# Kernel tuning notes

Hardware: AMD Instinct MI355X
Metric: run time of the kernel (lower is better)

Reference implementation:

```python
import jax, jax.numpy as jnp
import numpy as np

B, S, P, L, H = 64, 512, 32, 30, 768
FH = 1024  # fc_hidden_size


def setup_inputs() -> dict:
    key = jax.random.key(0)
    ks = jax.random.split(key, 8)
    token_embeddings = jax.random.normal(ks[0], (B, S, H), jnp.float32)
    pooler_output = jax.random.normal(ks[1], (B, H), jnp.float32)
    num_positions = jax.random.randint(ks[2], (B, P), 0, S)
    # labels: 0/1 codes, with trailing slots per example padded with -1 rows
    lab = jax.random.randint(ks[3], (B, P, L), 0, 2).astype(jnp.float32)
    valid = jax.random.randint(ks[4], (B, 1), 8, P + 1)  # num real slots per example
    row = jnp.arange(P)[None, :]
    lab = jnp.where((row < valid)[:, :, None], lab, -1.0)
    num_codes_labels = lab.reshape(B, P * L)
    W1 = jax.random.normal(ks[5], (2 * H, FH), jnp.float32) / np.sqrt(2 * H)
    b1 = jnp.zeros((FH,), jnp.float32)
    W2 = jax.random.normal(ks[6], (FH, FH // 2), jnp.float32) / np.sqrt(FH)
    b2 = jnp.zeros((FH // 2,), jnp.float32)
    W3 = jax.random.normal(ks[7], (FH // 2, L), jnp.float32) / np.sqrt(FH // 2)
    b3 = jnp.zeros((L,), jnp.float32)
    return {"token_embeddings": token_embeddings, "pooler_output": pooler_output,
            "num_positions": num_positions, "num_codes_labels": num_codes_labels,
            "W1": W1, "b1": b1, "W2": W2, "b2": b2, "W3": W3, "b3": b3}


def reference(token_embeddings, pooler_output, num_positions, num_codes_labels,
              W1, b1, W2, b2, W3, b3):
    # gather number-token hidden states: [B, P, H]
    p_hidden = jnp.take_along_axis(token_embeddings, num_positions[:, :, None], axis=1)
    feat = jnp.concatenate(
        [p_hidden, jnp.broadcast_to(pooler_output[:, None, :], p_hidden.shape)], axis=-1)
    # Batch_Net_CLS head. NOTE: original uses nn.LeakyReLU(True) -> negative_slope=1.0,
    # which is mathematically the identity, so the activations are omitted (faithful).
    h = feat @ W1 + b1
    h = h @ W2 + b2
    logits = h @ W3 + b3  # [B, P, L]

    labels = num_codes_labels.reshape(B, -1, L)
    pad_pre = jnp.any(labels != -1.0, axis=-1)  # [B, P] True for real slots
    mf = pad_pre.astype(jnp.float32)

    # BCEWithLogitsLoss over non-pad elements: softplus(x) - x*y, mean
    bce_elem = jax.nn.softplus(logits) - logits * labels
    bce_loss = jnp.sum(bce_elem * mf[:, :, None]) / (jnp.sum(mf) * L)

    binary = (jax.nn.sigmoid(logits) > 0.5).astype(jnp.float32)
    count_out = jnp.sum(binary, axis=-1)
    count_lab = jnp.sum(labels, axis=-1)
    count_loss = jnp.mean((count_out - count_lab) ** 2 * mf)

    # position loss: only slots where both counts are exactly 1 (single-hot)
    eq = (count_out == 1.0) & (count_lab == 1.0)
    pos_out = jnp.argmax(binary, axis=-1).astype(jnp.float32)
    pos_lab = jnp.argmax(labels, axis=-1).astype(jnp.float32)
    n_eq = jnp.sum(eq.astype(jnp.float32))
    pos_sum = jnp.sum((pos_out - pos_lab) ** 2 * eq.astype(jnp.float32))
    position_loss = jnp.where(n_eq > 0, pos_sum / jnp.maximum(n_eq, 1.0), 0.0)

    return bce_loss + 10.0 * count_loss + 5.0 * position_loss
```

## Files before the change

### kernel.cpp

```cpp
#include <hip/hip_runtime.h>
#include <cstddef>
#include <cstdint>

#define Mq   2048
#define Lq   30
#define N1q  1024
#define N2q  512
#define K1q  1536
#define Hq   768
#define NBLK 512

typedef float    f32x4 __attribute__((ext_vector_type(4)));
typedef _Float16 f16x8 __attribute__((ext_vector_type(8)));

#define GLD16(gptr, lptr) \
  __builtin_amdgcn_global_load_lds((const __attribute__((address_space(1))) void*)(gptr), \
                                   (__attribute__((address_space(3))) void*)(lptr), 16, 0, 0)

__device__ void transpose_tile(const float* __restrict__ src,
                               _Float16* __restrict__ dst,
                               int K, int N, int k0, int n0) {
  __shared__ float T[64][65];
  const int t = threadIdx.x;
  {
    const int kl = t >> 2, nc = (t & 3) * 16;
    const float* s = src + (size_t)(k0 + kl) * N + n0 + nc;
    float4 v0 = *(const float4*)s;
    float4 v1 = *(const float4*)(s + 4);
    float4 v2 = *(const float4*)(s + 8);
    float4 v3 = *(const float4*)(s + 12);
    T[nc + 0][kl] = v0.x; T[nc + 1][kl] = v0.y; T[nc + 2][kl] = v0.z; T[nc + 3][kl] = v0.w;
    T[nc + 4][kl] = v1.x; T[nc + 5][kl] = v1.y; T[nc + 6][kl] = v1.z; T[nc + 7][kl] = v1.w;
    T[nc + 8][kl] = v2.x; T[nc + 9][kl] = v2.y; T[nc +10][kl] = v2.z; T[nc +11][kl] = v2.w;
    T[nc +12][kl] = v3.x; T[nc +13][kl] = v3.y; T[nc +14][kl] = v3.z; T[nc +15][kl] = v3.w;
  }
  __syncthreads();
  {
    const int nl = t >> 2, kc = (t & 3) * 16;
    __align__(16) _Float16 tmp[16];
    #pragma unroll
    for (int i = 0; i < 16; ++i) tmp[i] = (_Float16)T[nl][kc + i];
    _Float16* d = dst + (size_t)(n0 + nl) * K + k0 + kc;
    *(uint4*)d       = *(const uint4*)tmp;
    *(uint4*)(d + 8) = *(const uint4*)(tmp + 8);
  }
}

__global__ __launch_bounds__(256)
void prep_all(const float* __restrict__ tok, const float* __restrict__ pool,
              const int* __restrict__ npos, const float* __restrict__ W1,
              const float* __restrict__ W2, const float* __restrict__ W3,
              _Float16* __restrict__ A1, _Float16* __restrict__ W1T,
              _Float16* __restrict__ W2T, float* __restrict__ W3T) {
  const int bid = blockIdx.x, tid = threadIdx.x;
  if (bid < 256) {
    const int q = tid >> 5, l32 = tid & 31;
    const int m = bid * 8 + q;
    const int bI = m >> 5, p = m & 31;
    const int pos = npos[bI * 32 + p];
    const float* src1 = tok + ((size_t)bI * 512 + pos) * Hq;
    const float* src2 = pool + (size_t)bI * Hq;
    _Float16* dst = A1 + (size_t)m * K1q;
    for (int g = l32; g < 384; g += 32) {
      const float* s = (g < 192) ? (src1 + g * 4) : (src2 + (g - 192) * 4);
      float4 v = *(const float4*)s;
      __align__(8) _Float16 o[4] = {(_Float16)v.x, (_Float16)v.y, (_Float16)v.z, (_Float16)v.w};
      *(uint2*)(dst + g * 4) = *(const uint2*)o;
    }
  } else if (bid < 640) {
    const int idx = bid - 256;
    transpose_tile(W1, W1T, K1q, N1q, (idx / 16) * 64, (idx % 16) * 64);
  } else if (bid < 768) {
    const int idx = bid - 640;
    transpose_tile(W2, W2T, N1q, N2q, (idx / 8) * 64, (idx % 8) * 64);
  } else {
    const int g = (bid - 768) * 256 + tid;
    for (int idx = g; idx < N2q * Lq; idx += 16 * 256) {
      const int k = idx / Lq, c = idx - k * Lq;
      W3T[(size_t)c * N2q + k] = W3[idx];
    }
  }
}

__global__ __launch_bounds__(256)
void gemm1_k(const _Float16* __restrict__ A, const _Float16* __restrict__ BT,
             const float* __restrict__ b1, _Float16* __restrict__ C1) {
  __shared__ _Float16 As[2][64 * 64];
  __shared__ _Float16 Bs[2][64 * 64];
  const int tid = threadIdx.x, w = tid >> 6, lane = tid & 63;
  const int n0 = blockIdx.x * 64, m0 = blockIdx.y * 64;
  const int ml = lane & 15, g4 = lane >> 4;
  const int wm = (w >> 1) * 32, wn = (w & 1) * 32;
  const int lr = lane >> 3, lc = lane & 7;

  f32x4 acc[2][2];
  #pragma unroll
  for (int i = 0; i < 2; ++i)
    #pragma unroll
    for (int j = 0; j < 2; ++j)
      #pragma unroll
      for (int r = 0; r < 4; ++r) acc[i][j][r] = 0.f;

  auto stage = [&](int it, int b) {
    const int kt = it * 64;
    #pragma unroll
    for (int t = 0; t < 2; ++t) {
      const int r  = w * 16 + t * 8 + lr;
      const int cs = lc ^ (r & 7);
      GLD16(A  + (size_t)(m0 + r) * K1q + kt + cs * 8, &As[b][(w * 16 + t * 8) * 64]);
      GLD16(BT + (size_t)(n0 + r) * K1q + kt + cs * 8, &Bs[b][(w * 16 + t * 8) * 64]);
    }
  };

  stage(0, 0);
  __syncthreads();
  #pragma unroll 1
  for (int it = 0; it < 24; ++it) {
    const int cur = it & 1;
    if (it < 23) stage(it + 1, cur ^ 1);
    f16x8 af[2][2], bf[2][2];
    #pragma unroll
    for (int i = 0; i < 2; ++i) {
      const int ar = wm + i * 16 + ml;
      const int br = wn + i * 16 + ml;
      #pragma unroll
      for (int ks = 0; ks < 2; ++ks) {
        af[i][ks] = *(const f16x8*)&As[cur][ar * 64 + (((ks * 4 + g4) ^ (ar & 7)) << 3)];
        bf[i][ks] = *(const f16x8*)&Bs[cur][br * 64 + (((ks * 4 + g4) ^ (br & 7)) << 3)];
      }
    }
    #pragma unroll
    for (int i = 0; i < 2; ++i)
      #pragma unroll
      for (int j = 0; j < 2; ++j)
        #pragma unroll
        for (int ks = 0; ks < 2; ++ks)
          acc[i][j] = __builtin_amdgcn_mfma_f32_16x16x32_f16(bf[j][ks], af[i][ks], acc[i][j], 0, 0, 0);
    __syncthreads();
  }

  #pragma unroll
  for (int i = 0; i < 2; ++i) {
    const int row = m0 + wm + i * 16 + ml;
    #pragma unroll
    for (int j = 0; j < 2; ++j) {
      const int col = n0 + wn + j * 16 + g4 * 4;
      const float4 bv = *(const float4*)(b1 + col);
      __align__(8) _Float16 o[4] = {(_Float16)(acc[i][j][0] + bv.x),
                                    (_Float16)(acc[i][j][1] + bv.y),
                                    (_Float16)(acc[i][j][2] + bv.z),
                                    (_Float16)(acc[i][j][3] + bv.w)};
      *(uint2*)(C1 + (size_t)row * N1q + col) = *(const uint2*)o;
    }
  }
}

__global__ __launch_bounds__(256)
void gemm2_k(const _Float16* __restrict__ A, const _Float16* __restrict__ BT,
             const float* __restrict__ b2, float* __restrict__ C2) {
  __shared__ _Float16 As[2][32 * 64];
  __shared__ _Float16 Bs[2][64 * 64];
  const int tid = threadIdx.x, w = tid >> 6, lane = tid & 63;
  const int n0 = blockIdx.x * 64, m0 = blockIdx.y * 32;
  const int ml = lane & 15, g4 = lane >> 4;
  const int wm = (w & 1) * 16, wn = (w >> 1) * 32;
  const int lr = lane >> 3, lc = lane & 7;

  f32x4 acc[2];
  #pragma unroll
  for (int j = 0; j < 2; ++j)
    #pragma unroll
    for (int r = 0; r < 4; ++r) acc[j][r] = 0.f;

  auto stage = [&](int it, int b) {
    const int kt = it * 64;
    {
      const int r  = w * 8 + lr;
      const int cs = lc ^ (r & 7);
      GLD16(A + (size_t)(m0 + r) * N1q + kt + cs * 8, &As[b][(w * 8) * 64]);
    }
    #pragma unroll
    for (int t = 0; t < 2; ++t) {
      const int r  = w * 16 + t * 8 + lr;
      const int cs = lc ^ (r & 7);
      GLD16(BT + (size_t)(n0 + r) * N1q + kt + cs * 8, &Bs[b][(w * 16 + t * 8) * 64]);
    }
  };

  stage(0, 0);
  __syncthreads();
  #pragma unroll 1
  for (int it = 0; it < 16; ++it) {
    const int cur = it & 1;
    if (it < 15) stage(it + 1, cur ^ 1);
    f16x8 af[2], bf[2][2];
    {
      const int ar = wm + ml;
      #pragma unroll
      for (int ks = 0; ks < 2; ++ks)
        af[ks] = *(const f16x8*)&As[cur][ar * 64 + (((ks * 4 + g4) ^ (ar & 7)) << 3)];
    }
    #pragma unroll
    for (int j = 0; j < 2; ++j) {
      const int br = wn + j * 16 + ml;
      #pragma unroll
      for (int ks = 0; ks < 2; ++ks)
        bf[j][ks] = *(const f16x8*)&Bs[cur][br * 64 + (((ks * 4 + g4) ^ (br & 7)) << 3)];
    }
    #pragma unroll
    for (int j = 0; j < 2; ++j)
      #pragma unroll
      for (int ks = 0; ks < 2; ++ks)
        acc[j] = __builtin_amdgcn_mfma_f32_16x16x32_f16(bf[j][ks], af[ks], acc[j], 0, 0, 0);
    __syncthreads();
  }

  const int row = m0 + wm + ml;
  #pragma unroll
  for (int j = 0; j < 2; ++j) {
    const int col = n0 + wn + j * 16 + g4 * 4;
    const float4 bv = *(const float4*)(b2 + col);
    float4 o;
    o.x = acc[j][0] + bv.x; o.y = acc[j][1] + bv.y;
    o.z = acc[j][2] + bv.z; o.w = acc[j][3] + bv.w;
    *(float4*)(C2 + (size_t)row * N2q + col) = o;
  }
}

__global__ __launch_bounds__(256)
void loss_kernel(const float* __restrict__ C2, const float* __restrict__ W3T,
                 const float* __restrict__ b3, const float* __restrict__ labels,
                 float* __restrict__ part) {
  __shared__ float hrow[4][512];
  __shared__ float red[4][5];
  const int tid = threadIdx.x, w = tid >> 6, lane = tid & 63;
  const int m = blockIdx.x * 4 + w;

  {
    const int k = lane * 8;
    const float* cp = C2 + (size_t)m * N2q + k;
    *(float4*)&hrow[w][k]     = *(const float4*)cp;
    *(float4*)&hrow[w][k + 4] = *(const float4*)(cp + 4);
  }
  __syncthreads();

  const int c  = lane & 31;
  const int kh = lane >> 5;
  float a0 = 0.f, a1 = 0.f, a2 = 0.f, a3 = 0.f;
  if (c < Lq) {
    const float* hp = hrow[w] + kh * 256;
    const float* wp = W3T + (size_t)c * N2q + kh * 256;
    #pragma unroll 4
    for (int i = 0; i < 256; i += 4) {
      const float4 wv = *(const float4*)(wp + i);
      a0 = fmaf(hp[i],     wv.x, a0);
      a1 = fmaf(hp[i + 1], wv.y, a1);
      a2 = fmaf(hp[i + 2], wv.z, a2);
      a3 = fmaf(hp[i + 3], wv.w, a3);
    }
  }
  float a = (a0 + a1) + (a2 + a3);
  a += __shfl_xor(a, 32);

  const bool act = lane < Lq;
  float logit = 0.f, lab = 0.f;
  if (act) {
    logit = a + b3[lane];
    lab = labels[(size_t)m * Lq + lane];
  }

  const unsigned long long validmask = __ballot(act && lab != -1.0f);
  const unsigned long long outmask   = __ballot(act && logit > 0.0f);
  const unsigned long long labmask   = __ballot(act && lab == 1.0f);
  const bool valid = (validmask != 0ULL);
  const int count_out = __popcll(outmask);
  const int count_lab = __popcll(labmask);

  float bce = 0.f;
  if (act && valid) {
    const float x = logit;
    bce = fmaxf(x, 0.f) + log1pf(expf(-fabsf(x))) - x * lab;
  }
  bce += __shfl_xor(bce, 16); bce += __shfl_xor(bce, 8);
  bce += __shfl_xor(bce, 4);  bce += __shfl_xor(bce, 2);
  bce += __shfl_xor(bce, 1);

  if (lane == 0) {
    float pb = 0.f, pv = 0.f, pc = 0.f, pe = 0.f, pp = 0.f;
    if (valid) {
      pb = bce; pv = 1.f;
      const float d = (float)count_out - (float)count_lab;
      pc = d * d;
    }
    if (count_out == 1 && count_lab == 1) {
      const float po = (float)(__ffsll((long long)outmask) - 1);
      const float pl = (float)(__ffsll((long long)labmask) - 1);
      pe = 1.f;
      const float dp = po - pl;
      pp = dp * dp;
    }
    red[w][0] = pb; red[w][1] = pv; red[w][2] = pc; red[w][3] = pe; red[w][4] = pp;
  }
  __syncthreads();
  if (tid < 5) {
    part[blockIdx.x * 5 + tid] =
        red[0][tid] + red[1][tid] + red[2][tid] + red[3][tid];
  }
}

__global__ __launch_bounds__(256)
void finalize_kernel(const float* __restrict__ part, float* __restrict__ out) {
  __shared__ float red[32][5];
  const int t = threadIdx.x;
  if (t < 160) {
    const int j = t % 5, grp = t / 5;
    float s = 0.f;
    for (int i = grp; i < NBLK; i += 32) s += part[i * 5 + j];
    red[grp][j] = s;
  }
  __syncthreads();
  if (t == 0) {
    float t0 = 0.f, t1 = 0.f, t2 = 0.f, t3 = 0.f, t4 = 0.f;
    #pragma unroll
    for (int g = 0; g < 32; ++g) {
      t0 += red[g][0]; t1 += red[g][1]; t2 += red[g][2];
      t3 += red[g][3]; t4 += red[g][4];
    }
    const float bce = t0 / (t1 * (float)Lq);
    const float cnt = 10.0f * t2 / (float)Mq;
    const float pos = (t3 > 0.f) ? 5.0f * t4 / fmaxf(t3, 1.0f) : 0.f;
    out[0] = bce + cnt + pos;
  }
}

extern "C" void kernel_launch(void* const* d_in, const int* in_sizes, int n_in,
                              void* d_out, int out_size, void* d_ws, size_t ws_size,
                              hipStream_t stream) {
  const float* tok    = (const float*)d_in[0];
  const float* pool   = (const float*)d_in[1];
  const int*   npos   = (const int*)  d_in[2];
  const float* labels = (const float*)d_in[3];
  const float* W1     = (const float*)d_in[4];
  const float* b1     = (const float*)d_in[5];
  const float* W2     = (const float*)d_in[6];
  const float* b2     = (const float*)d_in[7];
  const float* W3     = (const float*)d_in[8];
  const float* b3     = (const float*)d_in[9];
  float* out = (float*)d_out;

  char* ws = (char*)d_ws;
  _Float16* A1   = (_Float16*)(ws + 0x00000000);
  _Float16* W1T  = (_Float16*)(ws + 0x00600000);
  _Float16* W2T  = (_Float16*)(ws + 0x00900000);
  _Float16* C1   = (_Float16*)(ws + 0x00A00000);
  float*    C2   = (float*)   (ws + 0x00E00000);
  float*    part = (float*)   (ws + 0x01200000);
  float*    W3T  = (float*)   (ws + 0x01210000);

  prep_all<<<784, 256, 0, stream>>>(tok, pool, npos, W1, W2, W3, A1, W1T, W2T, W3T);
  gemm1_k<<<dim3(16, 32), 256, 0, stream>>>(A1, W1T, b1, C1);
  gemm2_k<<<dim3(8, 64), 256, 0, stream>>>(C1, W2T, b2, C2);
  loss_kernel<<<NBLK, 256, 0, stream>>>(C2, W3T, b3, labels, part);
  finalize_kernel<<<1, 256, 0, stream>>>(part, out);
}
```

Baseline: 200.8 us.

## Fold W2 and W3 into one matrix and drop the second GEMM

Because the head has no nonlinearity, W2·W3 and b2·W3+b3 are precomputed inside the prep kernel, giving a 1024x30 matrix and an effective bias. This removes the gemm2 kernel launch and its 2048x1024x512 MFMA work, along with the C2 intermediate. The loss kernel now does a 1024-long dot product per logit from the fp16 C1 activations. The precompute does a strided scalar read of W3 per thread, and the extra folding may shift rounding slightly compared with the previous fp16 path.

```diff
diff --git a/kernel.cpp b/kernel.cpp
--- a/kernel.cpp
+++ b/kernel.cpp
@@ -50,8 +50,9 @@
 void prep_all(const float* __restrict__ tok, const float* __restrict__ pool,
               const int* __restrict__ npos, const float* __restrict__ W1,
               const float* __restrict__ W2, const float* __restrict__ W3,
+              const float* __restrict__ b2, const float* __restrict__ b3,
               _Float16* __restrict__ A1, _Float16* __restrict__ W1T,
-              _Float16* __restrict__ W2T, float* __restrict__ W3T) {
+              float* __restrict__ W23T, float* __restrict__ beff) {
   const int bid = blockIdx.x, tid = threadIdx.x;
   if (bid < 256) {
     const int q = tid >> 5, l32 = tid & 31;
@@ -70,14 +71,35 @@
   } else if (bid < 640) {
     const int idx = bid - 256;
     transpose_tile(W1, W1T, K1q, N1q, (idx / 16) * 64, (idx % 16) * 64);
-  } else if (bid < 768) {
-    const int idx = bid - 640;
-    transpose_tile(W2, W2T, N1q, N2q, (idx / 8) * 64, (idx % 8) * 64);
+  } else if (bid < 760) {
+    const int idx = (bid - 640) * 256 + tid;
+    const int k = idx / Lq, c = idx - k * Lq;
+    const float* w2r = W2 + (size_t)k * N2q;
+    float s0 = 0.f, s1 = 0.f, s2 = 0.f, s3 = 0.f;
+    #pragma unroll 4
+    for (int j = 0; j < N2q; j += 4) {
+      const float4 wv = *(const float4*)(w2r + j);
+      s0 = fmaf(wv.x, W3[(size_t)(j)     * Lq + c], s0);
+      s1 = fmaf(wv.y, W3[(size_t)(j + 1) * Lq + c], s1);
+      s2 = fmaf(wv.z, W3[(size_t)(j + 2) * Lq + c], s2);
+      s3 = fmaf(wv.w, W3[(size_t)(j + 3) * Lq + c], s3);
+    }
+    W23T[(size_t)c * N1q + k] = (s0 + s1) + (s2 + s3);
   } else {
-    const int g = (bid - 768) * 256 + tid;
-    for (int idx = g; idx < N2q * Lq; idx += 16 * 256) {
-      const int k = idx / Lq, c = idx - k * Lq;
-      W3T[(size_t)c * N2q + k] = W3[idx];
+    __shared__ float R[8][32];
+    const int c = tid % Lq, jc = tid / Lq;
+    float s = 0.f;
+    if (tid < 240) {
+      for (int j = jc * 64; j < jc * 64 + 64; ++j)
+        s = fmaf(b2[j], W3[(size_t)j * Lq + c], s);
+      R[jc][c] = s;
+    }
+    __syncthreads();
+    if (tid < Lq) {
+      float t0 = b3[tid];
+      #pragma unroll
+      for (int g = 0; g < 8; ++g) t0 += R[g][tid];
+      beff[tid] = t0;
     }
   }
 }
@@ -156,91 +178,24 @@
 }
 
 __global__ __launch_bounds__(256)
-void gemm2_k(const _Float16* __restrict__ A, const _Float16* __restrict__ BT,
-             const float* __restrict__ b2, float* __restrict__ C2) {
-  __shared__ _Float16 As[2][32 * 64];
-  __shared__ _Float16 Bs[2][64 * 64];
-  const int tid = threadIdx.x, w = tid >> 6, lane = tid & 63;
-  const int n0 = blockIdx.x * 64, m0 = blockIdx.y * 32;
-  const int ml = lane & 15, g4 = lane >> 4;
-  const int wm = (w & 1) * 16, wn = (w >> 1) * 32;
-  const int lr = lane >> 3, lc = lane & 7;
-
-  f32x4 acc[2];
-  #pragma unroll
-  for (int j = 0; j < 2; ++j)
-    #pragma unroll
-    for (int r = 0; r < 4; ++r) acc[j][r] = 0.f;
-
-  auto stage = [&](int it, int b) {
-    const int kt = it * 64;
-    {
-      const int r  = w * 8 + lr;
-      const int cs = lc ^ (r & 7);
-      GLD16(A + (size_t)(m0 + r) * N1q + kt + cs * 8, &As[b][(w * 8) * 64]);
-    }
-    #pragma unroll
-    for (int t = 0; t < 2; ++t) {
-      const int r  = w * 16 + t * 8 + lr;
-      const int cs = lc ^ (r & 7);
-      GLD16(BT + (size_t)(n0 + r) * N1q + kt + cs * 8, &Bs[b][(w * 16 + t * 8) * 64]);
-    }
-  };
-
-  stage(0, 0);
-  __syncthreads();
-  #pragma unroll 1
-  for (int it = 0; it < 16; ++it) {
-    const int cur = it & 1;
-    if (it < 15) stage(it + 1, cur ^ 1);
-    f16x8 af[2], bf[2][2];
-    {
-      const int ar = wm + ml;
-      #pragma unroll
-      for (int ks = 0; ks < 2; ++ks)
-        af[ks] = *(const f16x8*)&As[cur][ar * 64 + (((ks * 4 + g4) ^ (ar & 7)) << 3)];
-    }
-    #pragma unroll
-    for (int j = 0; j < 2; ++j) {
-      const int br = wn + j * 16 + ml;
-      #pragma unroll
-      for (int ks = 0; ks < 2; ++ks)
-        bf[j][ks] = *(const f16x8*)&Bs[cur][br * 64 + (((ks * 4 + g4) ^ (br & 7)) << 3)];
-    }
-    #pragma unroll
-    for (int j = 0; j < 2; ++j)
-      #pragma unroll
-      for (int ks = 0; ks < 2; ++ks)
-        acc[j] = __builtin_amdgcn_mfma_f32_16x16x32_f16(bf[j][ks], af[ks], acc[j], 0, 0, 0);
-    __syncthreads();
-  }
-
-  const int row = m0 + wm + ml;
-  #pragma unroll
-  for (int j = 0; j < 2; ++j) {
-    const int col = n0 + wn + j * 16 + g4 * 4;
-    const float4 bv = *(const float4*)(b2 + col);
-    float4 o;
-    o.x = acc[j][0] + bv.x; o.y = acc[j][1] + bv.y;
-    o.z = acc[j][2] + bv.z; o.w = acc[j][3] + bv.w;
-    *(float4*)(C2 + (size_t)row * N2q + col) = o;
-  }
-}
-
-__global__ __launch_bounds__(256)
-void loss_kernel(const float* __restrict__ C2, const float* __restrict__ W3T,
-                 const float* __restrict__ b3, const float* __restrict__ labels,
+void loss_kernel(const _Float16* __restrict__ C1, const float* __restrict__ W23T,
+                 const float* __restrict__ beff, const float* __restrict__ labels,
                  float* __restrict__ part) {
-  __shared__ float hrow[4][512];
+  __shared__ float hrow[4][1024];
   __shared__ float red[4][5];
   const int tid = threadIdx.x, w = tid >> 6, lane = tid & 63;
   const int m = blockIdx.x * 4 + w;
 
   {
-    const int k = lane * 8;
-    const float* cp = C2 + (size_t)m * N2q + k;
-    *(float4*)&hrow[w][k]     = *(const float4*)cp;
-    *(float4*)&hrow[w][k + 4] = *(const float4*)(cp + 4);
+    const int k = lane * 16;
+    const _Float16* cp = C1 + (size_t)m * N1q + k;
+    f16x8 v0 = *(const f16x8*)cp;
+    f16x8 v1 = *(const f16x8*)(cp + 8);
+    #pragma unroll
+    for (int e = 0; e < 8; ++e) {
+      hrow[w][k + e]     = (float)v0[e];
+      hrow[w][k + 8 + e] = (float)v1[e];
+    }
   }
   __syncthreads();
 
@@ -248,10 +203,10 @@
   const int kh = lane >> 5;
   float a0 = 0.f, a1 = 0.f, a2 = 0.f, a3 = 0.f;
   if (c < Lq) {
-    const float* hp = hrow[w] + kh * 256;
-    const float* wp = W3T + (size_t)c * N2q + kh * 256;
+    const float* hp = hrow[w] + kh * 512;
+    const float* wp = W23T + (size_t)c * N1q + kh * 512;
     #pragma unroll 4
-    for (int i = 0; i < 256; i += 4) {
+    for (int i = 0; i < 512; i += 4) {
       const float4 wv = *(const float4*)(wp + i);
       a0 = fmaf(hp[i],     wv.x, a0);
       a1 = fmaf(hp[i + 1], wv.y, a1);
@@ -265,7 +220,7 @@
   const bool act = lane < Lq;
   float logit = 0.f, lab = 0.f;
   if (act) {
-    logit = a + b3[lane];
+    logit = a + beff[lane];
     lab = labels[(size_t)m * Lq + lane];
   }
 
@@ -351,15 +306,14 @@
   char* ws = (char*)d_ws;
   _Float16* A1   = (_Float16*)(ws + 0x00000000);
   _Float16* W1T  = (_Float16*)(ws + 0x00600000);
-  _Float16* W2T  = (_Float16*)(ws + 0x00900000);
-  _Float16* C1   = (_Float16*)(ws + 0x00A00000);
-  float*    C2   = (float*)   (ws + 0x00E00000);
-  float*    part = (float*)   (ws + 0x01200000);
-  float*    W3T  = (float*)   (ws + 0x01210000);
-
-  prep_all<<<784, 256, 0, stream>>>(tok, pool, npos, W1, W2, W3, A1, W1T, W2T, W3T);
+  _Float16* C1   = (_Float16*)(ws + 0x00900000);
+  float*    W23T = (float*)   (ws + 0x00D00000);
+  float*    beff = (float*)   (ws + 0x00D20000);
+  float*    part = (float*)   (ws + 0x00D30000);
+
+  prep_all<<<761, 256, 0, stream>>>(tok, pool, npos, W1, W2, W3, b2, b3,
+                                    A1, W1T, W23T, beff);
   gemm1_k<<<dim3(16, 32), 256, 0, stream>>>(A1, W1T, b1, C1);
-  gemm2_k<<<dim3(8, 64), 256, 0, stream>>>(C1, W2T, b2, C2);
-  loss_kernel<<<NBLK, 256, 0, stream>>>(C2, W3T, b3, labels, part);
+  loss_kernel<<<NBLK, 256, 0, stream>>>(C1, W23T, beff, labels, part);
   finalize_kernel<<<1, 256, 0, stream>>>(part, out);
 }
```

Measured after the change: 213.3 us. 6.2% more time.
